# Kernel optimization log

Hardware: AMD Instinct MI355X
Metric: run time of the kernel (lower is better)

Reference implementation:

```python
import jax, jax.numpy as jnp
import numpy as np

OUT, IN, B = 11008, 4096, 32

def setup_inputs() -> dict:
    key = jax.random.key(0)
    k1, k2, k3, k4 = jax.random.split(key, 4)
    x = jax.random.normal(k1, (B, IN), dtype=jnp.float32)
    # ternary weights in {-1, 0, +1}, stored as int (int8 semantics)
    weight_q = jax.random.randint(k2, (OUT, IN), -1, 2, dtype=jnp.int32)
    # per-row positive scale (fp16 in torch, cast to fp32 at dequant time)
    weight_scale = jax.random.uniform(k3, (OUT, 1), dtype=jnp.float32, minval=0.01, maxval=1.0)
    bias = jax.random.normal(k4, (OUT,), dtype=jnp.float32)
    return {"x": x, "weight_q": weight_q, "weight_scale": weight_scale, "bias": bias}

def reference(x, weight_q, weight_scale, bias):
    # dequantize_2bit: int8 ternary * per-row scale -> fp32 weight [OUT, IN]
    W = weight_q.astype(jnp.float32) * weight_scale.astype(jnp.float32)
    # F.linear: x @ W.T + bias
    return jnp.einsum('bi,oi->bo', x.astype(jnp.float32), W) + bias
```

## Files before the change

kernel.cpp:

```cpp
#include <hip/hip_runtime.h>

#define OUT_N 11008
#define IN_K  4096
#define BATCH 32
#define SEGS  8
#define KSEG  (IN_K / SEGS)
#define OPB   64
#define XSTRIDE 520

typedef __attribute__((ext_vector_type(8))) short short8;
typedef __attribute__((ext_vector_type(4))) float float4v;

__global__ __launch_bounds__(256) void prep_kernel(
    const float* __restrict__ x, const float* __restrict__ bias,
    unsigned short* __restrict__ xb, float* __restrict__ out)
{
    int i = blockIdx.x * 256 + threadIdx.x;
    if (i < BATCH * IN_K) {
        unsigned u = __builtin_bit_cast(unsigned, x[i]);
        unsigned r = u + 0x7FFFu + ((u >> 16) & 1u);
        xb[i] = (unsigned short)(r >> 16);
    }
    if (i < BATCH * OUT_N) {
        out[i] = bias[i % OUT_N];
    }
}

__device__ __forceinline__ unsigned pkbf16(float fhi, float flo) {
    return __builtin_amdgcn_perm(__builtin_bit_cast(unsigned, fhi),
                                 __builtin_bit_cast(unsigned, flo),
                                 0x07060302u);
}

__global__ __launch_bounds__(256, 4) void lin2bit_kernel(
    const int* __restrict__ wq, const float* __restrict__ scale,
    const unsigned short* __restrict__ xb, float* __restrict__ out)
{
    __shared__ unsigned short xs[BATCH][XSTRIDE];

    const int t    = threadIdx.x;
    const int lane = t & 63;
    const int wave = t >> 6;
    const int kseg = blockIdx.y * KSEG;

#pragma unroll
    for (int it = 0; it < 8; ++it) {
        int idx = it * 256 + t;
        int b   = idx >> 6;
        int k8  = (idx & 63) * 8;
        uint4 v = *reinterpret_cast<const uint4*>(xb + b * IN_K + kseg + k8);
        *reinterpret_cast<uint4*>(&xs[b][k8]) = v;
    }
    __syncthreads();

    const int quad = lane >> 4;
    const int l16  = lane & 15;
    const int o    = blockIdx.x * OPB + wave * 16 + l16;

    const int* __restrict__ wrow = wq + (size_t)o * IN_K + kseg + quad * 8;
    const unsigned short* xrow0 = &xs[l16][quad * 8];
    const unsigned short* xrow1 = &xs[l16 + 16][quad * 8];

    float4v acc0 = {0.f, 0.f, 0.f, 0.f};
    float4v acc1 = {0.f, 0.f, 0.f, 0.f};

#pragma unroll 4
    for (int ki = 0; ki < KSEG; ki += 32) {
        int4 w0 = *reinterpret_cast<const int4*>(wrow + ki);
        int4 w1 = *reinterpret_cast<const int4*>(wrow + ki + 4);
        uint4 bwu;
        bwu.x = pkbf16((float)w0.y, (float)w0.x);
        bwu.y = pkbf16((float)w0.w, (float)w0.z);
        bwu.z = pkbf16((float)w1.y, (float)w1.x);
        bwu.w = pkbf16((float)w1.w, (float)w1.z);
        short8 bfrag = __builtin_bit_cast(short8, bwu);

        short8 a0 = *reinterpret_cast<const short8*>(xrow0 + ki);
        short8 a1 = *reinterpret_cast<const short8*>(xrow1 + ki);

        acc0 = __builtin_amdgcn_mfma_f32_16x16x32_bf16(a0, bfrag, acc0, 0, 0, 0);
        acc1 = __builtin_amdgcn_mfma_f32_16x16x32_bf16(a1, bfrag, acc1, 0, 0, 0);
    }

    const float s = scale[o];
    const int b0 = quad * 4;
#pragma unroll
    for (int r = 0; r < 4; ++r) {
        unsafeAtomicAdd(out + (size_t)(b0 + r)      * OUT_N + o, s * acc0[r]);
        unsafeAtomicAdd(out + (size_t)(b0 + r + 16) * OUT_N + o, s * acc1[r]);
    }
}

extern "C" void kernel_launch(void* const* d_in, const int* in_sizes, int n_in,
                              void* d_out, int out_size, void* d_ws, size_t ws_size,
                              hipStream_t stream) {
    const float* x     = (const float*)d_in[0];
    const int*   wq    = (const int*)d_in[1];
    const float* scale = (const float*)d_in[2];
    const float* bias  = (const float*)d_in[3];
    float* out = (float*)d_out;
    unsigned short* xb = (unsigned short*)d_ws;

    prep_kernel<<<dim3((BATCH * OUT_N + 255) / 256), 256, 0, stream>>>(x, bias, xb, out);
    lin2bit_kernel<<<dim3(OUT_N / OPB, SEGS), 256, 0, stream>>>(wq, scale, xb, out);
}
```

Baseline: 256.3 us.

## Fuse x bf16 conversion into main kernel and software-pipeline weight loads

```diff
diff --git a/kernel.cpp b/kernel.cpp
--- a/kernel.cpp
+++ b/kernel.cpp
@@ -11,19 +11,17 @@
 typedef __attribute__((ext_vector_type(8))) short short8;
 typedef __attribute__((ext_vector_type(4))) float float4v;
 
-__global__ __launch_bounds__(256) void prep_kernel(
-    const float* __restrict__ x, const float* __restrict__ bias,
-    unsigned short* __restrict__ xb, float* __restrict__ out)
+__global__ __launch_bounds__(256) void init_kernel(
+    const float* __restrict__ bias, float* __restrict__ out)
 {
     int i = blockIdx.x * 256 + threadIdx.x;
-    if (i < BATCH * IN_K) {
-        unsigned u = __builtin_bit_cast(unsigned, x[i]);
-        unsigned r = u + 0x7FFFu + ((u >> 16) & 1u);
-        xb[i] = (unsigned short)(r >> 16);
-    }
-    if (i < BATCH * OUT_N) {
-        out[i] = bias[i % OUT_N];
-    }
+    if (i < BATCH * OUT_N) out[i] = bias[i % OUT_N];
+}
+
+__device__ __forceinline__ unsigned short f2bf(float f) {
+    unsigned u = __builtin_bit_cast(unsigned, f);
+    unsigned r = u + 0x7FFFu + ((u >> 16) & 1u);
+    return (unsigned short)(r >> 16);
 }
 
 __device__ __forceinline__ unsigned pkbf16(float fhi, float flo) {
@@ -34,7 +32,7 @@
 
 __global__ __launch_bounds__(256, 4) void lin2bit_kernel(
     const int* __restrict__ wq, const float* __restrict__ scale,
-    const unsigned short* __restrict__ xb, float* __restrict__ out)
+    const float* __restrict__ x, float* __restrict__ out)
 {
     __shared__ unsigned short xs[BATCH][XSTRIDE];
 
@@ -44,12 +42,13 @@
     const int kseg = blockIdx.y * KSEG;
 
 #pragma unroll
-    for (int it = 0; it < 8; ++it) {
+    for (int it = 0; it < 16; ++it) {
         int idx = it * 256 + t;
-        int b   = idx >> 6;
-        int k8  = (idx & 63) * 8;
-        uint4 v = *reinterpret_cast<const uint4*>(xb + b * IN_K + kseg + k8);
-        *reinterpret_cast<uint4*>(&xs[b][k8]) = v;
+        int b   = idx >> 7;
+        int k4  = idx & 127;
+        float4 v = *reinterpret_cast<const float4*>(x + b * IN_K + kseg + k4 * 4);
+        ushort4 h = { f2bf(v.x), f2bf(v.y), f2bf(v.z), f2bf(v.w) };
+        *reinterpret_cast<ushort4*>(&xs[b][k4 * 4]) = h;
     }
     __syncthreads();
 
@@ -57,30 +56,53 @@
     const int l16  = lane & 15;
     const int o    = blockIdx.x * OPB + wave * 16 + l16;
 
-    const int* __restrict__ wrow = wq + (size_t)o * IN_K + kseg + quad * 8;
+    const int* __restrict__ wp = wq + (size_t)o * IN_K + kseg + quad * 8;
     const unsigned short* xrow0 = &xs[l16][quad * 8];
     const unsigned short* xrow1 = &xs[l16 + 16][quad * 8];
 
     float4v acc0 = {0.f, 0.f, 0.f, 0.f};
     float4v acc1 = {0.f, 0.f, 0.f, 0.f};
 
-#pragma unroll 4
-    for (int ki = 0; ki < KSEG; ki += 32) {
-        int4 w0 = *reinterpret_cast<const int4*>(wrow + ki);
-        int4 w1 = *reinterpret_cast<const int4*>(wrow + ki + 4);
-        uint4 bwu;
-        bwu.x = pkbf16((float)w0.y, (float)w0.x);
-        bwu.y = pkbf16((float)w0.w, (float)w0.z);
-        bwu.z = pkbf16((float)w1.y, (float)w1.x);
-        bwu.w = pkbf16((float)w1.w, (float)w1.z);
-        short8 bfrag = __builtin_bit_cast(short8, bwu);
+    int4 p0 = *reinterpret_cast<const int4*>(wp);
+    int4 p1 = *reinterpret_cast<const int4*>(wp + 4);
+    int4 p2 = *reinterpret_cast<const int4*>(wp + 32);
+    int4 p3 = *reinterpret_cast<const int4*>(wp + 36);
 
-        short8 a0 = *reinterpret_cast<const short8*>(xrow0 + ki);
-        short8 a1 = *reinterpret_cast<const short8*>(xrow1 + ki);
+#define COMPUTE64(kbase, c0, c1, c2, c3)                                      \
+    do {                                                                      \
+        uint4 bw0;                                                            \
+        bw0.x = pkbf16((float)(c0).y, (float)(c0).x);                         \
+        bw0.y = pkbf16((float)(c0).w, (float)(c0).z);                         \
+        bw0.z = pkbf16((float)(c1).y, (float)(c1).x);                         \
+        bw0.w = pkbf16((float)(c1).w, (float)(c1).z);                         \
+        short8 bf0 = __builtin_bit_cast(short8, bw0);                         \
+        short8 a0 = *reinterpret_cast<const short8*>(xrow0 + (kbase));        \
+        short8 a1 = *reinterpret_cast<const short8*>(xrow1 + (kbase));        \
+        acc0 = __builtin_amdgcn_mfma_f32_16x16x32_bf16(a0, bf0, acc0, 0,0,0); \
+        acc1 = __builtin_amdgcn_mfma_f32_16x16x32_bf16(a1, bf0, acc1, 0,0,0); \
+        uint4 bw1;                                                            \
+        bw1.x = pkbf16((float)(c2).y, (float)(c2).x);                         \
+        bw1.y = pkbf16((float)(c2).w, (float)(c2).z);                         \
+        bw1.z = pkbf16((float)(c3).y, (float)(c3).x);                         \
+        bw1.w = pkbf16((float)(c3).w, (float)(c3).z);                         \
+        short8 bf1 = __builtin_bit_cast(short8, bw1);                         \
+        short8 a2 = *reinterpret_cast<const short8*>(xrow0 + (kbase) + 32);   \
+        short8 a3 = *reinterpret_cast<const short8*>(xrow1 + (kbase) + 32);   \
+        acc0 = __builtin_amdgcn_mfma_f32_16x16x32_bf16(a2, bf1, acc0, 0,0,0); \
+        acc1 = __builtin_amdgcn_mfma_f32_16x16x32_bf16(a3, bf1, acc1, 0,0,0); \
+    } while (0)
 
-        acc0 = __builtin_amdgcn_mfma_f32_16x16x32_bf16(a0, bfrag, acc0, 0, 0, 0);
-        acc1 = __builtin_amdgcn_mfma_f32_16x16x32_bf16(a1, bfrag, acc1, 0, 0, 0);
+#pragma unroll
+    for (int ki = 0; ki < KSEG - 64; ki += 64) {
+        int4 c0 = p0, c1 = p1, c2 = p2, c3 = p3;
+        p0 = *reinterpret_cast<const int4*>(wp + ki + 64);
+        p1 = *reinterpret_cast<const int4*>(wp + ki + 68);
+        p2 = *reinterpret_cast<const int4*>(wp + ki + 96);
+        p3 = *reinterpret_cast<const int4*>(wp + ki + 100);
+        COMPUTE64(ki, c0, c1, c2, c3);
     }
+    COMPUTE64(KSEG - 64, p0, p1, p2, p3);
+#undef COMPUTE64
 
     const float s = scale[o];
     const int b0 = quad * 4;
@@ -99,8 +121,7 @@
     const float* scale = (const float*)d_in[2];
     const float* bias  = (const float*)d_in[3];
     float* out = (float*)d_out;
-    unsigned short* xb = (unsigned short*)d_ws;
 
-    prep_kernel<<<dim3((BATCH * OUT_N + 255) / 256), 256, 0, stream>>>(x, bias, xb, out);
-    lin2bit_kernel<<<dim3(OUT_N / OPB, SEGS), 256, 0, stream>>>(wq, scale, xb, out);
+    init_kernel<<<dim3((BATCH * OUT_N + 255) / 256), 256, 0, stream>>>(bias, out);
+    lin2bit_kernel<<<dim3(OUT_N / OPB, SEGS), 256, 0, stream>>>(wq, scale, x, out);
 }
```

Result: slower. 262.7 us (+2.5%).

## Stage weights through LDS with coalesced loads and fuse x conversion into GEMV

Applied to the files above, without the earlier changes.

```diff
diff --git a/kernel.cpp b/kernel.cpp
--- a/kernel.cpp
+++ b/kernel.cpp
@@ -3,27 +3,25 @@
 #define OUT_N 11008
 #define IN_K  4096
 #define BATCH 32
-#define SEGS  8
+#define SEGS  16
 #define KSEG  (IN_K / SEGS)
 #define OPB   64
-#define XSTRIDE 520
+#define WSTR  (KSEG + 8)
 
 typedef __attribute__((ext_vector_type(8))) short short8;
 typedef __attribute__((ext_vector_type(4))) float float4v;
 
-__global__ __launch_bounds__(256) void prep_kernel(
-    const float* __restrict__ x, const float* __restrict__ bias,
-    unsigned short* __restrict__ xb, float* __restrict__ out)
+__global__ __launch_bounds__(256) void init_kernel(
+    const float* __restrict__ bias, float* __restrict__ out)
 {
     int i = blockIdx.x * 256 + threadIdx.x;
-    if (i < BATCH * IN_K) {
-        unsigned u = __builtin_bit_cast(unsigned, x[i]);
-        unsigned r = u + 0x7FFFu + ((u >> 16) & 1u);
-        xb[i] = (unsigned short)(r >> 16);
-    }
-    if (i < BATCH * OUT_N) {
-        out[i] = bias[i % OUT_N];
-    }
+    if (i < BATCH * OUT_N) out[i] = bias[i % OUT_N];
+}
+
+__device__ __forceinline__ unsigned short f2bf(float f) {
+    unsigned u = __builtin_bit_cast(unsigned, f);
+    unsigned r = u + 0x7FFFu + ((u >> 16) & 1u);
+    return (unsigned short)(r >> 16);
 }
 
 __device__ __forceinline__ unsigned pkbf16(float fhi, float flo) {
@@ -32,52 +30,57 @@
                                  0x07060302u);
 }
 
-__global__ __launch_bounds__(256, 4) void lin2bit_kernel(
+__global__ __launch_bounds__(256, 2) void lin2bit_kernel(
     const int* __restrict__ wq, const float* __restrict__ scale,
-    const unsigned short* __restrict__ xb, float* __restrict__ out)
+    const float* __restrict__ x, float* __restrict__ out)
 {
-    __shared__ unsigned short xs[BATCH][XSTRIDE];
+    __shared__ unsigned short wl[OPB][WSTR];
+    __shared__ unsigned short xs[BATCH][WSTR];
 
     const int t    = threadIdx.x;
     const int lane = t & 63;
     const int wave = t >> 6;
     const int kseg = blockIdx.y * KSEG;
+    const int o0   = blockIdx.x * OPB;
 
 #pragma unroll
     for (int it = 0; it < 8; ++it) {
         int idx = it * 256 + t;
         int b   = idx >> 6;
-        int k8  = (idx & 63) * 8;
-        uint4 v = *reinterpret_cast<const uint4*>(xb + b * IN_K + kseg + k8);
-        *reinterpret_cast<uint4*>(&xs[b][k8]) = v;
+        int k4  = idx & 63;
+        float4 v = *reinterpret_cast<const float4*>(x + b * IN_K + kseg + k4 * 4);
+        ushort4 h = { f2bf(v.x), f2bf(v.y), f2bf(v.z), f2bf(v.w) };
+        *reinterpret_cast<ushort4*>(&xs[b][k4 * 4]) = h;
+    }
+
+#pragma unroll
+    for (int r = 0; r < 16; ++r) {
+        const int rl = wave * 16 + r;
+        const int4 v = *reinterpret_cast<const int4*>(
+            wq + (size_t)(o0 + rl) * IN_K + kseg + lane * 4);
+        unsigned lo = pkbf16((float)v.y, (float)v.x);
+        unsigned hi = pkbf16((float)v.w, (float)v.z);
+        uint2 p = { lo, hi };
+        *reinterpret_cast<uint2*>(&wl[rl][lane * 4]) = p;
     }
     __syncthreads();
 
     const int quad = lane >> 4;
     const int l16  = lane & 15;
-    const int o    = blockIdx.x * OPB + wave * 16 + l16;
+    const int o    = o0 + wave * 16 + l16;
 
-    const int* __restrict__ wrow = wq + (size_t)o * IN_K + kseg + quad * 8;
+    const unsigned short* wrow = &wl[wave * 16 + l16][quad * 8];
     const unsigned short* xrow0 = &xs[l16][quad * 8];
     const unsigned short* xrow1 = &xs[l16 + 16][quad * 8];
 
     float4v acc0 = {0.f, 0.f, 0.f, 0.f};
     float4v acc1 = {0.f, 0.f, 0.f, 0.f};
 
-#pragma unroll 4
-    for (int ki = 0; ki < KSEG; ki += 32) {
-        int4 w0 = *reinterpret_cast<const int4*>(wrow + ki);
-        int4 w1 = *reinterpret_cast<const int4*>(wrow + ki + 4);
-        uint4 bwu;
-        bwu.x = pkbf16((float)w0.y, (float)w0.x);
-        bwu.y = pkbf16((float)w0.w, (float)w0.z);
-        bwu.z = pkbf16((float)w1.y, (float)w1.x);
-        bwu.w = pkbf16((float)w1.w, (float)w1.z);
-        short8 bfrag = __builtin_bit_cast(short8, bwu);
-
-        short8 a0 = *reinterpret_cast<const short8*>(xrow0 + ki);
-        short8 a1 = *reinterpret_cast<const short8*>(xrow1 + ki);
-
+#pragma unroll
+    for (int kt = 0; kt < KSEG / 32; ++kt) {
+        short8 bfrag = *reinterpret_cast<const short8*>(wrow + kt * 32);
+        short8 a0    = *reinterpret_cast<const short8*>(xrow0 + kt * 32);
+        short8 a1    = *reinterpret_cast<const short8*>(xrow1 + kt * 32);
         acc0 = __builtin_amdgcn_mfma_f32_16x16x32_bf16(a0, bfrag, acc0, 0, 0, 0);
         acc1 = __builtin_amdgcn_mfma_f32_16x16x32_bf16(a1, bfrag, acc1, 0, 0, 0);
     }
@@ -99,8 +102,7 @@
     const float* scale = (const float*)d_in[2];
     const float* bias  = (const float*)d_in[3];
     float* out = (float*)d_out;
-    unsigned short* xb = (unsigned short*)d_ws;
 
-    prep_kernel<<<dim3((BATCH * OUT_N + 255) / 256), 256, 0, stream>>>(x, bias, xb, out);
-    lin2bit_kernel<<<dim3(OUT_N / OPB, SEGS), 256, 0, stream>>>(wq, scale, xb, out);
+    init_kernel<<<dim3((BATCH * OUT_N + 255) / 256), 256, 0, stream>>>(bias, out);
+    lin2bit_kernel<<<dim3(OUT_N / OPB, SEGS), 256, 0, stream>>>(wq, scale, x, out);
 }
```

Result: no change. 255.8 us (-0.2%).
